# Performance work log

Measured on AMD Instinct MI355X. Metric: run time of the kernel, lower is better.

Reference implementation:

```python
import jax, jax.numpy as jnp
import numpy as np

B, S, H = 8, 2048, 768

def setup_inputs() -> dict:
    key = jax.random.key(0)
    ks = jax.random.split(key, 11)
    queries = jax.random.normal(ks[0], (B, S, H), dtype=jnp.float32)
    keys_ = jax.random.normal(ks[1], (B, S, H), dtype=jnp.float32)
    values = jax.random.normal(ks[2], (B, S, H), dtype=jnp.float32)
    coordinates = jax.random.uniform(ks[3], (B, S, 2), dtype=jnp.float32)
    scale = 1.0 / np.sqrt(H)
    Wq = jax.random.normal(ks[4], (H, H), dtype=jnp.float32) * scale
    bq = jnp.zeros((H,), dtype=jnp.float32)
    Wk = jax.random.normal(ks[5], (H, H), dtype=jnp.float32) * scale
    bk = jnp.zeros((H,), dtype=jnp.float32)
    Wv = jax.random.normal(ks[6], (H, H), dtype=jnp.float32) * scale
    bv = jnp.zeros((H,), dtype=jnp.float32)
    spatial_weight = jax.random.normal(ks[7], (1,), dtype=jnp.float32)
    return {"queries": queries, "keys": keys_, "values": values,
            "coordinates": coordinates, "Wq": Wq, "bq": bq, "Wk": Wk,
            "bk": bk, "Wv": Wv, "bv": bv, "spatial_weight": spatial_weight}

def _cdist(c):
    # c: [B, S, 2] -> pairwise euclidean distances [B, S, S]
    sq = jnp.sum(c * c, axis=-1)  # [B, S]
    d2 = sq[:, :, None] + sq[:, None, :] - 2.0 * jnp.einsum('bsd,btd->bst', c, c)
    return jnp.sqrt(jnp.maximum(d2, 1e-12))

def reference(queries, keys, values, coordinates, Wq, bq, Wk, bk, Wv, bv, spatial_weight):
    q = queries @ Wq.T + bq  # [B, S, H]
    k = keys @ Wk.T + bk
    v = values @ Wv.T + bv
    scores = jnp.einsum('bsh,bth->bst', q, k)          # [B, S, S]
    scores = scores - spatial_weight[0] * _cdist(coordinates)
    attn = jax.nn.softmax(scores, axis=-1)
    out = jnp.einsum('bst,bth->bsh', attn, v)          # [B, S, H]
    return out, attn
```

## Files before the change

kernel.cpp:

```cpp
#include <hip/hip_runtime.h>
#include <stdint.h>


typedef _Float16 half8 __attribute__((ext_vector_type(8)));
typedef _Float16 half4v __attribute__((ext_vector_type(4)));
typedef float f32x4 __attribute__((ext_vector_type(4)));

#define DEVI static __device__ __forceinline__

constexpr int B_ = 8, S_ = 2048, H_ = 768;
constexpr long NX = (long)B_ * S_ * H_;
constexpr long NW = (long)H_ * H_;

DEVI void glds16(const void* g, void* l) {
  __builtin_amdgcn_global_load_lds(
      (const __attribute__((address_space(1))) uint32_t*)g,
      (__attribute__((address_space(3))) uint32_t*)l, 16, 0, 0);
}

DEVI void stage_tile(const _Float16* gbase, int rowStride, _Float16* lds, int tid) {
#pragma unroll
  for (int seg = 0; seg < 2; ++seg) {
    int u = seg * 256 + tid;
    int r = u >> 2, c = u & 3;
    int sc = c ^ ((r >> 1) & 3);
    glds16(gbase + (long)r * rowStride + sc * 8, lds + ((u & ~63) << 3));
  }
}

DEVI half8 frag(const _Float16* lds, int m0, int lane) {
  int row = m0 + (lane & 15);
  int c = (lane >> 4) ^ ((row >> 1) & 3);
  return *(const half8*)(lds + row * 32 + c * 8);
}

__global__ __launch_bounds__(256) void k_split(
    const float* __restrict__ xq, const float* __restrict__ xk,
    const float* __restrict__ xv, const float* __restrict__ wq,
    const float* __restrict__ wk, const float* __restrict__ wv,
    _Float16* __restrict__ dst) {
  const long NX4 = NX / 4, NW4 = NW / 4, TOT = 3 * NX4 + 3 * NW4;
  for (long u = (long)blockIdx.x * blockDim.x + threadIdx.x; u < TOT;
       u += (long)gridDim.x * blockDim.x) {
    const float4* src;
    _Float16 *dh, *dl;
    long idx;
    if (u < 3 * NX4) {
      int z = (u >= 2 * NX4) ? 2 : (u >= NX4) ? 1 : 0;
      idx = u - (long)z * NX4;
      src = (const float4*)(z == 0 ? xq : z == 1 ? xk : xv);
      dh = dst + (long)z * 2 * NX;
      dl = dh + NX;
    } else {
      long t = u - 3 * NX4;
      int z = (t >= 2 * NW4) ? 2 : (t >= NW4) ? 1 : 0;
      idx = t - (long)z * NW4;
      src = (const float4*)(z == 0 ? wq : z == 1 ? wk : wv);
      dh = dst + 6 * NX + (long)z * 2 * NW;
      dl = dh + NW;
    }
    float4 x = src[idx];
    half4v hi, lo;
    hi[0] = (_Float16)x.x; lo[0] = (_Float16)(x.x - (float)hi[0]);
    hi[1] = (_Float16)x.y; lo[1] = (_Float16)(x.y - (float)hi[1]);
    hi[2] = (_Float16)x.z; lo[2] = (_Float16)(x.z - (float)hi[2]);
    hi[3] = (_Float16)x.w; lo[3] = (_Float16)(x.w - (float)hi[3]);
    *(half4v*)(dh + idx * 4) = hi;
    *(half4v*)(dl + idx * 4) = lo;
  }
}

__global__ __launch_bounds__(256, 2) void k_proj(
    const _Float16* __restrict__ scratch, const float* __restrict__ bq,
    const float* __restrict__ bk, const float* __restrict__ bv,
    _Float16* __restrict__ qh, _Float16* __restrict__ ql,
    _Float16* __restrict__ kh, _Float16* __restrict__ kl,
    _Float16* __restrict__ vT) {
  const int nt = blockIdx.x, mt = blockIdx.y, z = blockIdx.z;
  const int tid = threadIdx.x;
  const bool full = (z < 2);
  const _Float16* Xh = scratch + (long)z * 2 * NX;
  const _Float16* Xl = Xh + NX;
  const _Float16* Wh = scratch + 6 * NX + (long)z * 2 * NW;
  const _Float16* Wl = Wh + NW;
  const float* bias = (z == 0) ? bq : (z == 1) ? bk : bv;

  __shared__ _Float16 sm[2][4][4096];

  f32x4 acc[4][4] = {};

  const _Float16* Ah = Xh + (long)(mt * 128) * H_;
  const _Float16* Al = Xl + (long)(mt * 128) * H_;
  const _Float16* Bh = Wh + (long)(nt * 128) * H_;
  const _Float16* Bl = Wl + (long)(nt * 128) * H_;

  stage_tile(Ah, H_, sm[0][0], tid);
  stage_tile(Bh, H_, sm[0][2], tid);
  if (full) {
    stage_tile(Al, H_, sm[0][1], tid);
    stage_tile(Bl, H_, sm[0][3], tid);
  }
  __syncthreads();

  const int lane = tid & 63, wid = tid >> 6;
  const int wm = (wid >> 1) * 64, wn = (wid & 1) * 64;

  int cur = 0;
  for (int kk = 0; kk < 24; ++kk) {
    if (kk + 1 < 24) {
      int o = (kk + 1) * 32;
      stage_tile(Ah + o, H_, sm[cur ^ 1][0], tid);
      stage_tile(Bh + o, H_, sm[cur ^ 1][2], tid);
      if (full) {
        stage_tile(Al + o, H_, sm[cur ^ 1][1], tid);
        stage_tile(Bl + o, H_, sm[cur ^ 1][3], tid);
      }
    }
    half8 ah[4], bh[4];
#pragma unroll
    for (int i = 0; i < 4; ++i) ah[i] = frag(sm[cur][0], wm + i * 16, lane);
#pragma unroll
    for (int j = 0; j < 4; ++j) bh[j] = frag(sm[cur][2], wn + j * 16, lane);
#pragma unroll
    for (int i = 0; i < 4; ++i)
#pragma unroll
      for (int j = 0; j < 4; ++j)
        acc[i][j] = __builtin_amdgcn_mfma_f32_16x16x32_f16(ah[i], bh[j],
                                                           acc[i][j], 0, 0, 0);
    if (full) {
      half8 al[4], bl[4];
#pragma unroll
      for (int i = 0; i < 4; ++i) al[i] = frag(sm[cur][1], wm + i * 16, lane);
#pragma unroll
      for (int j = 0; j < 4; ++j) bl[j] = frag(sm[cur][3], wn + j * 16, lane);
#pragma unroll
      for (int i = 0; i < 4; ++i)
#pragma unroll
        for (int j = 0; j < 4; ++j) {
          acc[i][j] = __builtin_amdgcn_mfma_f32_16x16x32_f16(ah[i], bl[j],
                                                             acc[i][j], 0, 0, 0);
          acc[i][j] = __builtin_amdgcn_mfma_f32_16x16x32_f16(al[i], bh[j],
                                                             acc[i][j], 0, 0, 0);
        }
    }
    __syncthreads();
    cur ^= 1;
  }

  _Float16* oh = (z == 0) ? qh : kh;
  _Float16* ol = (z == 0) ? ql : kl;
#pragma unroll
  for (int i = 0; i < 4; ++i) {
    int m_t = wm + i * 16 + ((lane >> 4) << 2);
#pragma unroll
    for (int j = 0; j < 4; ++j) {
      int n_t = wn + j * 16 + (lane & 15);
      int gn = nt * 128 + n_t;
      float bs = bias[gn];
      if (z < 2) {
#pragma unroll
        for (int r = 0; r < 4; ++r) {
          long gm = (long)mt * 128 + m_t + r;
          float y = acc[i][j][r] + bs;
          _Float16 hi = (_Float16)y;
          oh[gm * H_ + gn] = hi;
          ol[gm * H_ + gn] = (_Float16)(y - (float)hi);
        }
      } else {
        int gmI = mt * 128 + m_t;
        int bb = gmI >> 11, t0 = gmI & 2047;
        half4v pk;
#pragma unroll
        for (int r = 0; r < 4; ++r) pk[r] = (_Float16)(acc[i][j][r] + bs);
        *(half4v*)&vT[((long)bb * H_ + gn) * S_ + t0] = pk;
      }
    }
  }
}

__global__ __launch_bounds__(256, 2) void k_scores(
    const _Float16* __restrict__ qh, const _Float16* __restrict__ ql,
    const _Float16* __restrict__ kh, const _Float16* __restrict__ kl,
    const float* __restrict__ coords, const float* __restrict__ sw,
    float* __restrict__ attn) {
  const int nt = blockIdx.x, mt = blockIdx.y, b = blockIdx.z;
  const int tid = threadIdx.x;
  __shared__ _Float16 sm[2][4][4096];
  __shared__ float cr[2][128], cc[2][128];

  if (tid < 128) {
    long gi = (long)b * S_ + mt * 128 + tid;
    cr[0][tid] = coords[gi * 2 + 0];
    cr[1][tid] = coords[gi * 2 + 1];
  } else {
    int t = tid - 128;
    long gj = (long)b * S_ + nt * 128 + t;
    cc[0][t] = coords[gj * 2 + 0];
    cc[1][t] = coords[gj * 2 + 1];
  }
  const float w = sw[0];

  f32x4 acc[4][4] = {};
  const long aoff = ((long)b * S_ + mt * 128) * H_;
  const long boff = ((long)b * S_ + nt * 128) * H_;
  const _Float16* Ah = qh + aoff;
  const _Float16* Al = ql + aoff;
  const _Float16* Bh = kh + boff;
  const _Float16* Bl = kl + boff;

  stage_tile(Ah, H_, sm[0][0], tid);
  stage_tile(Al, H_, sm[0][1], tid);
  stage_tile(Bh, H_, sm[0][2], tid);
  stage_tile(Bl, H_, sm[0][3], tid);
  __syncthreads();

  const int lane = tid & 63, wid = tid >> 6;
  const int wm = (wid >> 1) * 64, wn = (wid & 1) * 64;

  int cur = 0;
  for (int kk = 0; kk < 24; ++kk) {
    if (kk + 1 < 24) {
      int o = (kk + 1) * 32;
      stage_tile(Ah + o, H_, sm[cur ^ 1][0], tid);
      stage_tile(Al + o, H_, sm[cur ^ 1][1], tid);
      stage_tile(Bh + o, H_, sm[cur ^ 1][2], tid);
      stage_tile(Bl + o, H_, sm[cur ^ 1][3], tid);
    }
    half8 ah[4], al4[4], bh[4], bl4[4];
#pragma unroll
    for (int i = 0; i < 4; ++i) {
      ah[i] = frag(sm[cur][0], wm + i * 16, lane);
      al4[i] = frag(sm[cur][1], wm + i * 16, lane);
    }
#pragma unroll
    for (int j = 0; j < 4; ++j) {
      bh[j] = frag(sm[cur][2], wn + j * 16, lane);
      bl4[j] = frag(sm[cur][3], wn + j * 16, lane);
    }
#pragma unroll
    for (int i = 0; i < 4; ++i)
#pragma unroll
      for (int j = 0; j < 4; ++j) {
        acc[i][j] = __builtin_amdgcn_mfma_f32_16x16x32_f16(ah[i], bh[j],
                                                           acc[i][j], 0, 0, 0);
        acc[i][j] = __builtin_amdgcn_mfma_f32_16x16x32_f16(ah[i], bl4[j],
                                                           acc[i][j], 0, 0, 0);
        acc[i][j] = __builtin_amdgcn_mfma_f32_16x16x32_f16(al4[i], bh[j],
                                                           acc[i][j], 0, 0, 0);
      }
    __syncthreads();
    cur ^= 1;
  }

#pragma unroll
  for (int i = 0; i < 4; ++i) {
    int m_t = wm + i * 16 + ((lane >> 4) << 2);
#pragma unroll
    for (int j = 0; j < 4; ++j) {
      int n_t = wn + j * 16 + (lane & 15);
      float cjx = cc[0][n_t], cjy = cc[1][n_t];
      long rowbase = ((long)b * S_ + mt * 128 + m_t) * S_ + nt * 128 + n_t;
#pragma unroll
      for (int r = 0; r < 4; ++r) {
        float dx = cr[0][m_t + r] - cjx;
        float dy = cr[1][m_t + r] - cjy;
        float d = sqrtf(fmaxf(fmaf(dx, dx, dy * dy), 1e-12f));
        attn[rowbase + (long)r * S_] = acc[i][j][r] - w * d;
      }
    }
  }
}

__global__ __launch_bounds__(256) void k_rowsoft(float* __restrict__ attn) {
  const int wid = threadIdx.x >> 6, lane = threadIdx.x & 63;
  float* p = attn + ((long)blockIdx.x * 4 + wid) * S_;
  float4 v[8];
#pragma unroll
  for (int i = 0; i < 8; ++i) v[i] = ((const float4*)p)[i * 64 + lane];
  float m = -3.4e38f;
#pragma unroll
  for (int i = 0; i < 8; ++i)
    m = fmaxf(m, fmaxf(fmaxf(v[i].x, v[i].y), fmaxf(v[i].z, v[i].w)));
#pragma unroll
  for (int o = 32; o > 0; o >>= 1) m = fmaxf(m, __shfl_xor(m, o));
  float l = 0.f;
#pragma unroll
  for (int i = 0; i < 8; ++i) {
    v[i].x = __expf(v[i].x - m);
    v[i].y = __expf(v[i].y - m);
    v[i].z = __expf(v[i].z - m);
    v[i].w = __expf(v[i].w - m);
    l += (v[i].x + v[i].y) + (v[i].z + v[i].w);
  }
#pragma unroll
  for (int o = 32; o > 0; o >>= 1) l += __shfl_xor(l, o);
  const float rl = 1.0f / l;
#pragma unroll
  for (int i = 0; i < 8; ++i) {
    v[i].x *= rl; v[i].y *= rl; v[i].z *= rl; v[i].w *= rl;
    ((float4*)p)[i * 64 + lane] = v[i];
  }
}

__global__ __launch_bounds__(256, 2) void k_pv(
    const float* __restrict__ attn, const _Float16* __restrict__ vT,
    float* __restrict__ outp) {
  const int nt = blockIdx.x, mt = blockIdx.y, b = blockIdx.z;
  const int tid = threadIdx.x;
  __shared__ _Float16 sm[2][2][4096];
  f32x4 acc[4][4] = {};
  const float* Ab = attn + ((long)b * S_ + mt * 128) * S_;
  const _Float16* Bb = vT + ((long)b * H_ + nt * 128) * S_;
  const int lane = tid & 63, wid = tid >> 6;
  const int wm = (wid >> 1) * 64, wn = (wid & 1) * 64;

  stage_tile(Bb, S_, sm[0][1], tid);
#pragma unroll
  for (int seg = 0; seg < 2; ++seg) {
    int u = seg * 256 + tid, r = u >> 2, c = u & 3;
    int sc = c ^ ((r >> 1) & 3);
    const float4* s4 = (const float4*)(Ab + (long)r * S_ + sc * 8);
    float4 x0 = s4[0], x1 = s4[1];
    half8 h = {(_Float16)x0.x, (_Float16)x0.y, (_Float16)x0.z, (_Float16)x0.w,
               (_Float16)x1.x, (_Float16)x1.y, (_Float16)x1.z, (_Float16)x1.w};
    *(half8*)(&sm[0][0][r * 32 + c * 8]) = h;
  }
  __syncthreads();

  int cur = 0;
  for (int kk = 0; kk < 64; ++kk) {
    float4 x0a, x1a, x0b, x1b;
    const bool pre = (kk + 1 < 64);
    if (pre) {
      stage_tile(Bb + (kk + 1) * 32, S_, sm[cur ^ 1][1], tid);
      {
        int u = tid, r = u >> 2, sc = (u & 3) ^ ((r >> 1) & 3);
        const float4* s4 =
            (const float4*)(Ab + (long)r * S_ + (kk + 1) * 32 + sc * 8);
        x0a = s4[0]; x1a = s4[1];
      }
      {
        int u = 256 + tid, r = u >> 2, sc = (u & 3) ^ ((r >> 1) & 3);
        const float4* s4 =
            (const float4*)(Ab + (long)r * S_ + (kk + 1) * 32 + sc * 8);
        x0b = s4[0]; x1b = s4[1];
      }
    }
    half8 ah[4], bh[4];
#pragma unroll
    for (int i = 0; i < 4; ++i) ah[i] = frag(sm[cur][0], wm + i * 16, lane);
#pragma unroll
    for (int j = 0; j < 4; ++j) bh[j] = frag(sm[cur][1], wn + j * 16, lane);
#pragma unroll
    for (int i = 0; i < 4; ++i)
#pragma unroll
      for (int j = 0; j < 4; ++j)
        acc[i][j] = __builtin_amdgcn_mfma_f32_16x16x32_f16(ah[i], bh[j],
                                                           acc[i][j], 0, 0, 0);
    if (pre) {
      {
        int u = tid, r = u >> 2, c = u & 3;
        half8 h = {(_Float16)x0a.x, (_Float16)x0a.y, (_Float16)x0a.z,
                   (_Float16)x0a.w, (_Float16)x1a.x, (_Float16)x1a.y,
                   (_Float16)x1a.z, (_Float16)x1a.w};
        *(half8*)(&sm[cur ^ 1][0][r * 32 + c * 8]) = h;
      }
      {
        int u = 256 + tid, r = u >> 2, c = u & 3;
        half8 h = {(_Float16)x0b.x, (_Float16)x0b.y, (_Float16)x0b.z,
                   (_Float16)x0b.w, (_Float16)x1b.x, (_Float16)x1b.y,
                   (_Float16)x1b.z, (_Float16)x1b.w};
        *(half8*)(&sm[cur ^ 1][0][r * 32 + c * 8]) = h;
      }
    }
    __syncthreads();
    cur ^= 1;
  }

#pragma unroll
  for (int i = 0; i < 4; ++i) {
    int m_t = wm + i * 16 + ((lane >> 4) << 2);
#pragma unroll
    for (int j = 0; j < 4; ++j) {
      int n_t = wn + j * 16 + (lane & 15);
      int h = nt * 128 + n_t;
      long rowbase = (long)b * S_ + mt * 128 + m_t;
#pragma unroll
      for (int r = 0; r < 4; ++r) outp[(rowbase + r) * H_ + h] = acc[i][j][r];
    }
  }
}

extern "C" void kernel_launch(void* const* d_in, const int* in_sizes, int n_in,
                              void* d_out, int out_size, void* d_ws,
                              size_t ws_size, hipStream_t stream) {
  const float* xq = (const float*)d_in[0];
  const float* xk = (const float*)d_in[1];
  const float* xv = (const float*)d_in[2];
  const float* co = (const float*)d_in[3];
  const float* wq = (const float*)d_in[4];
  const float* bq = (const float*)d_in[5];
  const float* wk = (const float*)d_in[6];
  const float* bk = (const float*)d_in[7];
  const float* wv = (const float*)d_in[8];
  const float* bv = (const float*)d_in[9];
  const float* sw = (const float*)d_in[10];

  float* out = (float*)d_out;
  float* attn = out + NX;
  _Float16* scratch = (_Float16*)d_out;

  _Float16* qh = (_Float16*)d_ws;
  _Float16* ql = qh + NX;
  _Float16* kh = ql + NX;
  _Float16* kl = kh + NX;
  _Float16* vT = kl + NX;

  k_split<<<dim3(2048), 256, 0, stream>>>(xq, xk, xv, wq, wk, wv, scratch);
  k_proj<<<dim3(6, 128, 3), 256, 0, stream>>>(scratch, bq, bk, bv, qh, ql, kh,
                                              kl, vT);
  k_scores<<<dim3(16, 16, 8), 256, 0, stream>>>(qh, ql, kh, kl, co, sw, attn);
  k_rowsoft<<<dim3(4096), 256, 0, stream>>>(attn);
  k_pv<<<dim3(6, 16, 8), 256, 0, stream>>>(attn, vT, out);
}
```

Before: 557.8 us.

## Fuse fp32 hi/lo split into projection GEMM and feed PV with fp16 attention

```diff
diff --git a/kernel.cpp b/kernel.cpp
--- a/kernel.cpp
+++ b/kernel.cpp
@@ -11,6 +11,7 @@
 constexpr int B_ = 8, S_ = 2048, H_ = 768;
 constexpr long NX = (long)B_ * S_ * H_;
 constexpr long NW = (long)H_ * H_;
+constexpr long ATT = (long)B_ * S_ * S_;
 
 DEVI void glds16(const void* g, void* l) {
   __builtin_amdgcn_global_load_lds(
@@ -34,71 +35,59 @@
   return *(const half8*)(lds + row * 32 + c * 8);
 }
 
-__global__ __launch_bounds__(256) void k_split(
+DEVI void split8(const float4& x0, const float4& x1, half8& hi, half8& lo) {
+  float v[8] = {x0.x, x0.y, x0.z, x0.w, x1.x, x1.y, x1.z, x1.w};
+#pragma unroll
+  for (int k = 0; k < 8; ++k) {
+    hi[k] = (_Float16)v[k];
+    lo[k] = (_Float16)(v[k] - (float)hi[k]);
+  }
+}
+
+__global__ __launch_bounds__(256, 2) void k_proj_fused(
     const float* __restrict__ xq, const float* __restrict__ xk,
     const float* __restrict__ xv, const float* __restrict__ wq,
     const float* __restrict__ wk, const float* __restrict__ wv,
-    _Float16* __restrict__ dst) {
-  const long NX4 = NX / 4, NW4 = NW / 4, TOT = 3 * NX4 + 3 * NW4;
-  for (long u = (long)blockIdx.x * blockDim.x + threadIdx.x; u < TOT;
-       u += (long)gridDim.x * blockDim.x) {
-    const float4* src;
-    _Float16 *dh, *dl;
-    long idx;
-    if (u < 3 * NX4) {
-      int z = (u >= 2 * NX4) ? 2 : (u >= NX4) ? 1 : 0;
-      idx = u - (long)z * NX4;
-      src = (const float4*)(z == 0 ? xq : z == 1 ? xk : xv);
-      dh = dst + (long)z * 2 * NX;
-      dl = dh + NX;
-    } else {
-      long t = u - 3 * NX4;
-      int z = (t >= 2 * NW4) ? 2 : (t >= NW4) ? 1 : 0;
-      idx = t - (long)z * NW4;
-      src = (const float4*)(z == 0 ? wq : z == 1 ? wk : wv);
-      dh = dst + 6 * NX + (long)z * 2 * NW;
-      dl = dh + NW;
-    }
-    float4 x = src[idx];
-    half4v hi, lo;
-    hi[0] = (_Float16)x.x; lo[0] = (_Float16)(x.x - (float)hi[0]);
-    hi[1] = (_Float16)x.y; lo[1] = (_Float16)(x.y - (float)hi[1]);
-    hi[2] = (_Float16)x.z; lo[2] = (_Float16)(x.z - (float)hi[2]);
-    hi[3] = (_Float16)x.w; lo[3] = (_Float16)(x.w - (float)hi[3]);
-    *(half4v*)(dh + idx * 4) = hi;
-    *(half4v*)(dl + idx * 4) = lo;
-  }
-}
-
-__global__ __launch_bounds__(256, 2) void k_proj(
-    const _Float16* __restrict__ scratch, const float* __restrict__ bq,
-    const float* __restrict__ bk, const float* __restrict__ bv,
-    _Float16* __restrict__ qh, _Float16* __restrict__ ql,
-    _Float16* __restrict__ kh, _Float16* __restrict__ kl,
-    _Float16* __restrict__ vT) {
+    const float* __restrict__ bq, const float* __restrict__ bk,
+    const float* __restrict__ bv, _Float16* __restrict__ qh,
+    _Float16* __restrict__ ql, _Float16* __restrict__ kh,
+    _Float16* __restrict__ kl, _Float16* __restrict__ vT) {
   const int nt = blockIdx.x, mt = blockIdx.y, z = blockIdx.z;
   const int tid = threadIdx.x;
   const bool full = (z < 2);
-  const _Float16* Xh = scratch + (long)z * 2 * NX;
-  const _Float16* Xl = Xh + NX;
-  const _Float16* Wh = scratch + 6 * NX + (long)z * 2 * NW;
-  const _Float16* Wl = Wh + NW;
+  const float* X = (z == 0) ? xq : (z == 1) ? xk : xv;
+  const float* W = (z == 0) ? wq : (z == 1) ? wk : wv;
   const float* bias = (z == 0) ? bq : (z == 1) ? bk : bv;
 
   __shared__ _Float16 sm[2][4][4096];
-
   f32x4 acc[4][4] = {};
 
-  const _Float16* Ah = Xh + (long)(mt * 128) * H_;
-  const _Float16* Al = Xl + (long)(mt * 128) * H_;
-  const _Float16* Bh = Wh + (long)(nt * 128) * H_;
-  const _Float16* Bl = Wl + (long)(nt * 128) * H_;
-
-  stage_tile(Ah, H_, sm[0][0], tid);
-  stage_tile(Bh, H_, sm[0][2], tid);
-  if (full) {
-    stage_tile(Al, H_, sm[0][1], tid);
-    stage_tile(Bl, H_, sm[0][3], tid);
+  const float* Ab = X + (long)(mt * 128) * H_;
+  const float* Bb = W + (long)(nt * 128) * H_;
+
+  int rr[2], cc_[2], scc[2];
+#pragma unroll
+  for (int seg = 0; seg < 2; ++seg) {
+    int u = seg * 256 + tid;
+    rr[seg] = u >> 2;
+    cc_[seg] = u & 3;
+    scc[seg] = cc_[seg] ^ ((rr[seg] >> 1) & 3);
+  }
+
+#pragma unroll
+  for (int seg = 0; seg < 2; ++seg) {
+    const float4* sa = (const float4*)(Ab + (long)rr[seg] * H_ + scc[seg] * 8);
+    const float4* sb = (const float4*)(Bb + (long)rr[seg] * H_ + scc[seg] * 8);
+    half8 hi, lo, bhi, blo;
+    split8(sa[0], sa[1], hi, lo);
+    split8(sb[0], sb[1], bhi, blo);
+    int off = rr[seg] * 32 + cc_[seg] * 8;
+    *(half8*)(&sm[0][0][off]) = hi;
+    *(half8*)(&sm[0][2][off]) = bhi;
+    if (full) {
+      *(half8*)(&sm[0][1][off]) = lo;
+      *(half8*)(&sm[0][3][off]) = blo;
+    }
   }
   __syncthreads();
 
@@ -107,13 +96,18 @@
 
   int cur = 0;
   for (int kk = 0; kk < 24; ++kk) {
-    if (kk + 1 < 24) {
+    const bool pre = (kk + 1 < 24);
+    float4 pa[2][2], pb[2][2];
+    if (pre) {
       int o = (kk + 1) * 32;
-      stage_tile(Ah + o, H_, sm[cur ^ 1][0], tid);
-      stage_tile(Bh + o, H_, sm[cur ^ 1][2], tid);
-      if (full) {
-        stage_tile(Al + o, H_, sm[cur ^ 1][1], tid);
-        stage_tile(Bl + o, H_, sm[cur ^ 1][3], tid);
+#pragma unroll
+      for (int seg = 0; seg < 2; ++seg) {
+        const float4* sa =
+            (const float4*)(Ab + (long)rr[seg] * H_ + o + scc[seg] * 8);
+        pa[seg][0] = sa[0]; pa[seg][1] = sa[1];
+        const float4* sb =
+            (const float4*)(Bb + (long)rr[seg] * H_ + o + scc[seg] * 8);
+        pb[seg][0] = sb[0]; pb[seg][1] = sb[1];
       }
     }
     half8 ah[4], bh[4];
@@ -143,6 +137,21 @@
                                                              acc[i][j], 0, 0, 0);
         }
     }
+    if (pre) {
+#pragma unroll
+      for (int seg = 0; seg < 2; ++seg) {
+        half8 hi, lo, bhi, blo;
+        split8(pa[seg][0], pa[seg][1], hi, lo);
+        split8(pb[seg][0], pb[seg][1], bhi, blo);
+        int off = rr[seg] * 32 + cc_[seg] * 8;
+        *(half8*)(&sm[cur ^ 1][0][off]) = hi;
+        *(half8*)(&sm[cur ^ 1][2][off]) = bhi;
+        if (full) {
+          *(half8*)(&sm[cur ^ 1][1][off]) = lo;
+          *(half8*)(&sm[cur ^ 1][3][off]) = blo;
+        }
+      }
+    }
     __syncthreads();
     cur ^= 1;
   }
@@ -157,7 +166,7 @@
       int n_t = wn + j * 16 + (lane & 15);
       int gn = nt * 128 + n_t;
       float bs = bias[gn];
-      if (z < 2) {
+      if (full) {
 #pragma unroll
         for (int r = 0; r < 4; ++r) {
           long gm = (long)mt * 128 + m_t + r;
@@ -271,9 +280,12 @@
   }
 }
 
-__global__ __launch_bounds__(256) void k_rowsoft(float* __restrict__ attn) {
+__global__ __launch_bounds__(256) void k_rowsoft(float* __restrict__ attn,
+                                                 _Float16* __restrict__ a16) {
   const int wid = threadIdx.x >> 6, lane = threadIdx.x & 63;
-  float* p = attn + ((long)blockIdx.x * 4 + wid) * S_;
+  long row = (long)blockIdx.x * 4 + wid;
+  float* p = attn + row * S_;
+  _Float16* p16 = a16 + row * S_;
   float4 v[8];
 #pragma unroll
   for (int i = 0; i < 8; ++i) v[i] = ((const float4*)p)[i * 64 + lane];
@@ -299,52 +311,32 @@
   for (int i = 0; i < 8; ++i) {
     v[i].x *= rl; v[i].y *= rl; v[i].z *= rl; v[i].w *= rl;
     ((float4*)p)[i * 64 + lane] = v[i];
-  }
-}
-
-__global__ __launch_bounds__(256, 2) void k_pv(
-    const float* __restrict__ attn, const _Float16* __restrict__ vT,
+    half4v h = {(_Float16)v[i].x, (_Float16)v[i].y, (_Float16)v[i].z,
+                (_Float16)v[i].w};
+    ((half4v*)p16)[i * 64 + lane] = h;
+  }
+}
+
+__global__ __launch_bounds__(256, 2) void k_pv16(
+    const _Float16* __restrict__ a16, const _Float16* __restrict__ vT,
     float* __restrict__ outp) {
   const int nt = blockIdx.x, mt = blockIdx.y, b = blockIdx.z;
-  const int tid = threadIdx.x;
+  const int tid = threadIdx.x, lane = tid & 63, wid = tid >> 6;
+  const int wm = (wid >> 1) * 64, wn = (wid & 1) * 64;
   __shared__ _Float16 sm[2][2][4096];
   f32x4 acc[4][4] = {};
-  const float* Ab = attn + ((long)b * S_ + mt * 128) * S_;
+  const _Float16* Ab = a16 + ((long)b * S_ + mt * 128) * S_;
   const _Float16* Bb = vT + ((long)b * H_ + nt * 128) * S_;
-  const int lane = tid & 63, wid = tid >> 6;
-  const int wm = (wid >> 1) * 64, wn = (wid & 1) * 64;
-
+
+  stage_tile(Ab, S_, sm[0][0], tid);
   stage_tile(Bb, S_, sm[0][1], tid);
-#pragma unroll
-  for (int seg = 0; seg < 2; ++seg) {
-    int u = seg * 256 + tid, r = u >> 2, c = u & 3;
-    int sc = c ^ ((r >> 1) & 3);
-    const float4* s4 = (const float4*)(Ab + (long)r * S_ + sc * 8);
-    float4 x0 = s4[0], x1 = s4[1];
-    half8 h = {(_Float16)x0.x, (_Float16)x0.y, (_Float16)x0.z, (_Float16)x0.w,
-               (_Float16)x1.x, (_Float16)x1.y, (_Float16)x1.z, (_Float16)x1.w};
-    *(half8*)(&sm[0][0][r * 32 + c * 8]) = h;
-  }
   __syncthreads();
 
   int cur = 0;
   for (int kk = 0; kk < 64; ++kk) {
-    float4 x0a, x1a, x0b, x1b;
-    const bool pre = (kk + 1 < 64);
-    if (pre) {
+    if (kk + 1 < 64) {
+      stage_tile(Ab + (kk + 1) * 32, S_, sm[cur ^ 1][0], tid);
       stage_tile(Bb + (kk + 1) * 32, S_, sm[cur ^ 1][1], tid);
-      {
-        int u = tid, r = u >> 2, sc = (u & 3) ^ ((r >> 1) & 3);
-        const float4* s4 =
-            (const float4*)(Ab + (long)r * S_ + (kk + 1) * 32 + sc * 8);
-        x0a = s4[0]; x1a = s4[1];
-      }
-      {
-        int u = 256 + tid, r = u >> 2, sc = (u & 3) ^ ((r >> 1) & 3);
-        const float4* s4 =
-            (const float4*)(Ab + (long)r * S_ + (kk + 1) * 32 + sc * 8);
-        x0b = s4[0]; x1b = s4[1];
-      }
     }
     half8 ah[4], bh[4];
 #pragma unroll
@@ -357,22 +349,6 @@
       for (int j = 0; j < 4; ++j)
         acc[i][j] = __builtin_amdgcn_mfma_f32_16x16x32_f16(ah[i], bh[j],
                                                            acc[i][j], 0, 0, 0);
-    if (pre) {
-      {
-        int u = tid, r = u >> 2, c = u & 3;
-        half8 h = {(_Float16)x0a.x, (_Float16)x0a.y, (_Float16)x0a.z,
-                   (_Float16)x0a.w, (_Float16)x1a.x, (_Float16)x1a.y,
-                   (_Float16)x1a.z, (_Float16)x1a.w};
-        *(half8*)(&sm[cur ^ 1][0][r * 32 + c * 8]) = h;
-      }
-      {
-        int u = 256 + tid, r = u >> 2, c = u & 3;
-        half8 h = {(_Float16)x0b.x, (_Float16)x0b.y, (_Float16)x0b.z,
-                   (_Float16)x0b.w, (_Float16)x1b.x, (_Float16)x1b.y,
-                   (_Float16)x1b.z, (_Float16)x1b.w};
-        *(half8*)(&sm[cur ^ 1][0][r * 32 + c * 8]) = h;
-      }
-    }
     __syncthreads();
     cur ^= 1;
   }
@@ -408,18 +384,17 @@
 
   float* out = (float*)d_out;
   float* attn = out + NX;
-  _Float16* scratch = (_Float16*)d_out;
 
   _Float16* qh = (_Float16*)d_ws;
   _Float16* ql = qh + NX;
   _Float16* kh = ql + NX;
   _Float16* kl = kh + NX;
   _Float16* vT = kl + NX;
-
-  k_split<<<dim3(2048), 256, 0, stream>>>(xq, xk, xv, wq, wk, wv, scratch);
-  k_proj<<<dim3(6, 128, 3), 256, 0, stream>>>(scratch, bq, bk, bv, qh, ql, kh,
-                                              kl, vT);
+  _Float16* a16 = qh;
+
+  k_proj_fused<<<dim3(6, 128, 3), 256, 0, stream>>>(xq, xk, xv, wq, wk, wv, bq,
+                                                    bk, bv, qh, ql, kh, kl, vT);
   k_scores<<<dim3(16, 16, 8), 256, 0, stream>>>(qh, ql, kh, kl, co, sw, attn);
-  k_rowsoft<<<dim3(4096), 256, 0, stream>>>(attn);
-  k_pv<<<dim3(6, 16, 8), 256, 0, stream>>>(attn, vT, out);
-}
+  k_rowsoft<<<dim3(4096), 256, 0, stream>>>(attn, a16);
+  k_pv16<<<dim3(6, 16, 8), 256, 0, stream>>>(a16, vT, out);
+}
```

After: 537.2 us. 1.04x faster.
